# Optimization experiments

Hardware: AMD Instinct MI355X
Metric: run time of the kernel (lower is better)

Reference implementation:

```python
import jax, jax.numpy as jnp
import numpy as np

VOCAB = 50001; W2V = 300; S2V = 256; HID = 256; COUT = 256; NTAG = 4; NHEADS = 5
N_POSTS = 2048; SEQ = 64


def mha(x, wqkv, bqkv, wo, bo, h):
    # torch nn.MultiheadAttention (batch_first, eval mode, no mask)
    n, s, d = x.shape
    hd = d // h
    qkv = x @ wqkv.T + bqkv                      # [n, s, 3d]
    q, k, v = jnp.split(qkv, 3, axis=-1)
    rs = lambda t: t.reshape(n, s, h, hd).transpose(0, 2, 1, 3)  # [n, h, s, hd]
    q, k, v = rs(q), rs(k), rs(v)
    att = jax.nn.softmax(jnp.einsum('nhqd,nhkd->nhqk', q, k) * (hd ** -0.5), axis=-1)
    o = jnp.einsum('nhqk,nhkd->nhqd', att, v).transpose(0, 2, 1, 3).reshape(n, s, d)
    return o @ wo.T + bo


def gcn_conv(x, ei, w, b):
    n = x.shape[0]
    loops = jnp.arange(n)
    src = jnp.concatenate([ei[0], loops])
    dst = jnp.concatenate([ei[1], loops])
    deg = jax.ops.segment_sum(jnp.ones(dst.shape[0], dtype=x.dtype), dst, num_segments=n)
    dinv = jnp.where(deg > 0, jax.lax.rsqrt(deg), 0.0)
    norm = dinv[src] * dinv[dst]                 # [E+n]
    h = x @ w.T                                  # [n, out]
    return jax.ops.segment_sum(norm[:, None] * h[src], dst, num_segments=n) + b


def gcn_branch(x, ei, root, w1, b1, w2, b2):
    # GCN.forward: conv1 -> cat root feat -> relu -> conv2 -> relu -> cat conv1 root -> mean
    n = x.shape[0]
    c1 = gcn_conv(x, ei, w1, b1)                 # [n, HID]
    post_root = jnp.broadcast_to(x[root], (n, x.shape[1]))
    c2_in = jax.nn.relu(jnp.concatenate([c1, post_root], axis=1))
    c2 = jax.nn.relu(gcn_conv(c2_in, ei, w2, b2))
    c1_root = jnp.broadcast_to(c1[root], (n, c1.shape[1]))
    feat = jnp.concatenate([c1_root, c2], axis=1)  # [n, HID+COUT]
    return jnp.mean(feat, axis=0).reshape(1, -1)


def setup_inputs() -> dict:
    key = jax.random.key(0)
    ks = jax.random.split(key, 16)
    p = lambda i, shp, sc=0.02: jax.random.normal(ks[i], shp, dtype=jnp.float32) * sc
    return {
        'nodeText': jax.random.randint(ks[0], (N_POSTS, SEQ), 0, VOCAB),
        'edgeIndexTD': jax.random.randint(ks[1], (2, N_POSTS - 1), 0, N_POSTS),
        'edgeIndexBU': jax.random.randint(ks[2], (2, N_POSTS - 1), 0, N_POSTS),
        'threadIndex': 0,
        'mission': 1,
        'embed_w': p(3, (VOCAB, W2V), 1.0),
        'in_proj_w': p(4, (3 * W2V, W2V)),
        'in_proj_b': jnp.zeros((3 * W2V,), jnp.float32),
        'out_proj_w': p(5, (W2V, W2V)),
        'out_proj_b': jnp.zeros((W2V,), jnp.float32),
        's2v_w': p(6, (S2V, W2V)),
        's2v_b': jnp.zeros((S2V,), jnp.float32),
        'td_w1': p(7, (HID, S2V)), 'td_b1': jnp.zeros((HID,), jnp.float32),
        'td_w2': p(8, (COUT, HID + S2V)), 'td_b2': jnp.zeros((COUT,), jnp.float32),
        'bu_w1': p(9, (HID, S2V)), 'bu_b1': jnp.zeros((HID,), jnp.float32),
        'bu_w2': p(10, (COUT, HID + S2V)), 'bu_b2': jnp.zeros((COUT,), jnp.float32),
        'fc_w': p(11, (NTAG, (COUT + HID) * 2)),
        'fc_b': jnp.zeros((NTAG,), jnp.float32),
    }


def reference(nodeText, edgeIndexTD, edgeIndexBU, threadIndex, mission,
              embed_w, in_proj_w, in_proj_b, out_proj_w, out_proj_b,
              s2v_w, s2v_b, td_w1, td_b1, td_w2, td_b2,
              bu_w1, bu_b1, bu_w2, bu_b2, fc_w, fc_b):
    # ABGCN.forward, mission == 1 (rumor/BiGCN path), eval mode (dropout off)
    nf = embed_w[nodeText]                                  # [N, S, W2V]
    nf = mha(nf, in_proj_w, in_proj_b, out_proj_w, out_proj_b, NHEADS)
    nf = jnp.tanh(nf @ s2v_w.T + s2v_b)                     # [N, S, S2V]
    s2v = nf[:, 0, :]                                       # first token per post
    td = gcn_branch(s2v, edgeIndexTD, threadIndex, td_w1, td_b1, td_w2, td_b2)
    bu = gcn_branch(s2v, edgeIndexBU, threadIndex, bu_w1, bu_b1, bu_w2, bu_b2)
    return jnp.concatenate([td, bu], axis=1) @ fc_w.T + fc_b  # [1, NTAG]
```

## Files before the change

### kernel.cpp

```cpp
#include <hip/hip_runtime.h>

#define NPOSTS 2048
#define SEQ 64
#define W2V 300
#define NH 5
#define HD 60
#define S2VD 256
#define HIDD 256
#define NEDGE 2047

__global__ __launch_bounds__(320) void k_q(
    const int* __restrict__ nodeText, const float* __restrict__ embed_w,
    const float* __restrict__ Wqkv, const float* __restrict__ bqkv,
    float* __restrict__ Qout)
{
    const int r0 = blockIdx.x * 16;
    const int tid = threadIdx.x;
    __shared__ float sE[16][W2V];
    for (int i = tid; i < 16 * 75; i += 320) {
        int r = i / 75, c4 = (i % 75) * 4;
        int t = nodeText[(size_t)(r0 + r) * SEQ];
        const float4 v = *reinterpret_cast<const float4*>(embed_w + (size_t)t * W2V + c4);
        sE[r][c4] = v.x; sE[r][c4 + 1] = v.y; sE[r][c4 + 2] = v.z; sE[r][c4 + 3] = v.w;
    }
    __syncthreads();
    if (tid < W2V) {
        const float* wr = Wqkv + (size_t)tid * W2V;
        float acc[16];
        float b = bqkv[tid];
        #pragma unroll
        for (int r = 0; r < 16; ++r) acc[r] = b;
        for (int c = 0; c < W2V; ++c) {
            float wv = wr[c];
            #pragma unroll
            for (int r = 0; r < 16; ++r) acc[r] = fmaf(wv, sE[r][c], acc[r]);
        }
        #pragma unroll
        for (int r = 0; r < 16; ++r) Qout[(size_t)(r0 + r) * W2V + tid] = acc[r];
    }
}

__global__ __launch_bounds__(320) void k_u(
    const float* __restrict__ Q, const float* __restrict__ Wqkv, float* __restrict__ uout)
{
    const int r0 = blockIdx.x * 16;
    const int h = blockIdx.y;
    const int tid = threadIdx.x;
    __shared__ float sQ[16][HD];
    for (int i = tid; i < 16 * HD; i += 320) {
        int r = i / HD, d = i % HD;
        sQ[r][d] = Q[(size_t)(r0 + r) * W2V + h * HD + d];
    }
    __syncthreads();
    if (tid < W2V) {
        float acc[16];
        #pragma unroll
        for (int r = 0; r < 16; ++r) acc[r] = 0.f;
        const float* wb = Wqkv + (size_t)(W2V + h * HD) * W2V + tid;
        for (int d = 0; d < HD; ++d) {
            float wv = wb[(size_t)d * W2V];
            #pragma unroll
            for (int r = 0; r < 16; ++r) acc[r] = fmaf(wv, sQ[r][d], acc[r]);
        }
        #pragma unroll
        for (int r = 0; r < 16; ++r)
            uout[(size_t)(r0 + r) * (NH * W2V) + h * W2V + tid] = acc[r];
    }
}

__global__ __launch_bounds__(256) void k_att(
    const int* __restrict__ nodeText, const float* __restrict__ embed_w,
    float* __restrict__ ue)
{
    __shared__ float sEmb[SEQ][W2V + 1];
    __shared__ int   stoks[SEQ];
    __shared__ float ssc[NH * SEQ];

    const int p = blockIdx.x;
    const int tid = threadIdx.x;

    if (tid < SEQ) stoks[tid] = nodeText[p * SEQ + tid];
    __syncthreads();

    for (int idx = tid; idx < SEQ * 75; idx += 256) {
        int r = idx / 75, c4 = (idx % 75) * 4;
        const float4 v = *reinterpret_cast<const float4*>(embed_w + (size_t)stoks[r] * W2V + c4);
        float* dst = &sEmb[r][c4];
        dst[0] = v.x; dst[1] = v.y; dst[2] = v.z; dst[3] = v.w;
    }
    __syncthreads();

    const float* urow = ue + (size_t)p * (NH * W2V);
    for (int i = tid; i < NH * SEQ; i += 256) {
        int h = i / SEQ, j = i % SEQ;
        const float4* u4 = reinterpret_cast<const float4*>(urow + h * W2V);
        const float* er = sEmb[j];
        float acc = 0.f;
        for (int c4 = 0; c4 < 75; ++c4) {
            float4 u = u4[c4];
            int c = c4 * 4;
            acc = fmaf(u.x, er[c], acc);
            acc = fmaf(u.y, er[c + 1], acc);
            acc = fmaf(u.z, er[c + 2], acc);
            acc = fmaf(u.w, er[c + 3], acc);
        }
        ssc[i] = acc * 0.12909944487358056f;
    }
    __syncthreads();

    {
        const int wave = tid >> 6, lane = tid & 63;
        for (int h = wave; h < NH; h += 4) {
            float v = ssc[h * SEQ + lane];
            float m = v;
            #pragma unroll
            for (int off = 32; off > 0; off >>= 1) m = fmaxf(m, __shfl_xor(m, off));
            float e = expf(v - m);
            float s = e;
            #pragma unroll
            for (int off = 32; off > 0; off >>= 1) s += __shfl_xor(s, off);
            ssc[h * SEQ + lane] = e / s;
        }
    }
    __syncthreads();

    float* erow = ue + (size_t)p * (NH * W2V);
    for (int i = tid; i < NH * W2V; i += 256) {
        int h = i / W2V, c = i % W2V;
        const float* att = ssc + h * SEQ;
        float acc = 0.f;
        #pragma unroll 4
        for (int j = 0; j < SEQ; ++j) acc = fmaf(att[j], sEmb[j][c], acc);
        erow[i] = acc;
    }
}

__global__ __launch_bounds__(320) void k_oms(
    const float* __restrict__ e, const float* __restrict__ Wqkv, const float* __restrict__ bqkv,
    const float* __restrict__ Wo, const float* __restrict__ bo,
    const float* __restrict__ Ws, const float* __restrict__ bs,
    float* __restrict__ s2v_out)
{
    const int r0 = blockIdx.x * 8;
    const int tid = threadIdx.x;
    __shared__ float se[8][NH * W2V];
    __shared__ float so[8][W2V];
    __shared__ float sm[8][W2V];

    for (int i = tid; i < 8 * 375; i += 320) {
        int r = i / 375, c4 = (i % 375) * 4;
        const float4 v = *reinterpret_cast<const float4*>(e + (size_t)(r0 + r) * (NH * W2V) + c4);
        float* dst = &se[r][c4];
        dst[0] = v.x; dst[1] = v.y; dst[2] = v.z; dst[3] = v.w;
    }
    __syncthreads();

    if (tid < W2V) {
        const int h = tid / HD;
        const float* wr = Wqkv + (size_t)(2 * W2V + tid) * W2V;
        float acc[8];
        float b = bqkv[2 * W2V + tid];
        #pragma unroll
        for (int r = 0; r < 8; ++r) acc[r] = b;
        for (int c = 0; c < W2V; ++c) {
            float wv = wr[c];
            #pragma unroll
            for (int r = 0; r < 8; ++r) acc[r] = fmaf(wv, se[r][h * W2V + c], acc[r]);
        }
        #pragma unroll
        for (int r = 0; r < 8; ++r) so[r][tid] = acc[r];
    }
    __syncthreads();

    if (tid < W2V) {
        const float* wr = Wo + (size_t)tid * W2V;
        float acc[8];
        float b = bo[tid];
        #pragma unroll
        for (int r = 0; r < 8; ++r) acc[r] = b;
        for (int c = 0; c < W2V; ++c) {
            float wv = wr[c];
            #pragma unroll
            for (int r = 0; r < 8; ++r) acc[r] = fmaf(wv, so[r][c], acc[r]);
        }
        #pragma unroll
        for (int r = 0; r < 8; ++r) sm[r][tid] = acc[r];
    }
    __syncthreads();

    if (tid < S2VD) {
        const float* wr = Ws + (size_t)tid * W2V;
        float acc[8];
        float b = bs[tid];
        #pragma unroll
        for (int r = 0; r < 8; ++r) acc[r] = b;
        for (int c = 0; c < W2V; ++c) {
            float wv = wr[c];
            #pragma unroll
            for (int r = 0; r < 8; ++r) acc[r] = fmaf(wv, sm[r][c], acc[r]);
        }
        #pragma unroll
        for (int r = 0; r < 8; ++r)
            s2v_out[(size_t)(r0 + r) * S2VD + tid] = tanhf(acc[r]);
    }
}


__global__ __launch_bounds__(256) void k_deg(
    const int* __restrict__ eiTD, const int* __restrict__ eiBU, int* __restrict__ deg)
{
    const int b = blockIdx.y;
    const int* ei = b ? eiBU : eiTD;
    int e = blockIdx.x * 256 + threadIdx.x;
    if (e < NEDGE) atomicAdd(&deg[b * NPOSTS + ei[NEDGE + e]], 1);
}

__global__ __launch_bounds__(256) void k_gemm1(
    const float* __restrict__ x, const float* __restrict__ wtd, const float* __restrict__ wbu,
    float* __restrict__ hout)
{
    const int b = blockIdx.y;
    const float* w = b ? wbu : wtd;
    float* outp = hout + (size_t)b * NPOSTS * HIDD;
    const int r0 = blockIdx.x * 16;
    const int tid = threadIdx.x;
    __shared__ float sx[16][S2VD];
    for (int i = tid; i < 16 * S2VD; i += 256)
        sx[i / S2VD][i % S2VD] = x[(size_t)(r0 + i / S2VD) * S2VD + (i % S2VD)];
    __syncthreads();
    float acc[16];
    #pragma unroll
    for (int r = 0; r < 16; ++r) acc[r] = 0.f;
    const float* wr = w + (size_t)tid * S2VD;
    for (int c = 0; c < S2VD; ++c) {
        float wv = wr[c];
        #pragma unroll
        for (int r = 0; r < 16; ++r) acc[r] = fmaf(wv, sx[r][c], acc[r]);
    }
    #pragma unroll
    for (int r = 0; r < 16; ++r) outp[(size_t)(r0 + r) * HIDD + tid] = acc[r];
}

__global__ __launch_bounds__(256) void k_gemm2(
    const float* __restrict__ c1, const float* __restrict__ w2td, const float* __restrict__ w2bu,
    const float* __restrict__ rootv, float* __restrict__ hout)
{
    const int b = blockIdx.y;
    const float* w = b ? w2bu : w2td;
    const float* xin = c1 + (size_t)b * NPOSTS * HIDD;
    float* outp = hout + (size_t)b * NPOSTS * HIDD;
    const int r0 = blockIdx.x * 16;
    const int tid = threadIdx.x;
    __shared__ float sx[16][HIDD];
    for (int i = tid; i < 16 * HIDD; i += 256)
        sx[i / HIDD][i % HIDD] = fmaxf(xin[(size_t)(r0 + i / HIDD) * HIDD + (i % HIDD)], 0.f);
    __syncthreads();
    float acc[16];
    const float rv = rootv[b * HIDD + tid];
    #pragma unroll
    for (int r = 0; r < 16; ++r) acc[r] = rv;
    const float* wr = w + (size_t)tid * 512;
    for (int c = 0; c < HIDD; ++c) {
        float wv = wr[c];
        #pragma unroll
        for (int r = 0; r < 16; ++r) acc[r] = fmaf(wv, sx[r][c], acc[r]);
    }
    #pragma unroll
    for (int r = 0; r < 16; ++r) outp[(size_t)(r0 + r) * HIDD + tid] = acc[r];
}

__global__ __launch_bounds__(256) void k_init(
    const float* __restrict__ h, const float* __restrict__ btd, const float* __restrict__ bbu,
    const int* __restrict__ deg, float* __restrict__ cout_)
{
    const int b = blockIdx.y, n = blockIdx.x, tid = threadIdx.x;
    const float* bias = b ? bbu : btd;
    const float* hb = h + (size_t)b * NPOSTS * HIDD;
    float* cb = cout_ + (size_t)b * NPOSTS * HIDD;
    float dinv = 1.f / (float)(deg[b * NPOSTS + n] + 1);
    cb[(size_t)n * HIDD + tid] = bias[tid] + hb[(size_t)n * HIDD + tid] * dinv;
}

__global__ __launch_bounds__(256) void k_scat(
    const int* __restrict__ eiTD, const int* __restrict__ eiBU,
    const float* __restrict__ h, const int* __restrict__ deg, float* __restrict__ cacc)
{
    const int b = blockIdx.y, e = blockIdx.x, tid = threadIdx.x;
    const int* ei = b ? eiBU : eiTD;
    const int s = ei[e], d = ei[NEDGE + e];
    const int* dg = deg + b * NPOSTS;
    float norm = rsqrtf((float)(dg[s] + 1)) * rsqrtf((float)(dg[d] + 1));
    const float* hb = h + (size_t)b * NPOSTS * HIDD;
    float* cb = cacc + (size_t)b * NPOSTS * HIDD;
    atomicAdd(&cb[(size_t)d * HIDD + tid], norm * hb[(size_t)s * HIDD + tid]);
}

__global__ __launch_bounds__(256) void k_root(
    const float* __restrict__ s2v, const float* __restrict__ c1,
    const float* __restrict__ w2td, const float* __restrict__ w2bu,
    const int* __restrict__ rootPtr, float* __restrict__ rootv, float* __restrict__ c1root)
{
    const int b = blockIdx.y, tid = threadIdx.x;
    const float* w2 = b ? w2bu : w2td;
    const int root = rootPtr[0];
    __shared__ float sx[S2VD];
    sx[tid] = fmaxf(s2v[(size_t)root * S2VD + tid], 0.f);
    __syncthreads();
    const float* cb = c1 + (size_t)b * NPOSTS * HIDD;
    c1root[b * HIDD + tid] = cb[(size_t)root * HIDD + tid];
    const float* wr = w2 + (size_t)tid * 512 + 256;
    float acc = 0.f;
    #pragma unroll 4
    for (int c = 0; c < S2VD; ++c) acc = fmaf(wr[c], sx[c], acc);
    rootv[b * HIDD + tid] = acc;
}

__global__ __launch_bounds__(256) void k_reduce(
    const float* __restrict__ cacc, float* __restrict__ msum)
{
    const int b = blockIdx.y, tid = threadIdx.x;
    const int base = blockIdx.x * 32;
    const float* cb = cacc + (size_t)b * NPOSTS * HIDD;
    float local = 0.f;
    #pragma unroll 4
    for (int r = 0; r < 32; ++r) local += fmaxf(cb[(size_t)(base + r) * HIDD + tid], 0.f);
    atomicAdd(&msum[b * HIDD + tid], local);
}

__global__ __launch_bounds__(256) void k_final(
    const float* __restrict__ c1root, const float* __restrict__ msum,
    const float* __restrict__ fc_w, const float* __restrict__ fc_b, float* __restrict__ outp)
{
    const int tid = threadIdx.x;
    __shared__ float sf[1024];
    for (int k = tid; k < 1024; k += 256) {
        int seg = k >> 8, idx = k & 255;
        float v;
        if (seg == 0)      v = c1root[idx];
        else if (seg == 1) v = msum[idx] * (1.f / (float)NPOSTS);
        else if (seg == 2) v = c1root[256 + idx];
        else               v = msum[256 + idx] * (1.f / (float)NPOSTS);
        sf[k] = v;
    }
    __syncthreads();
    const int t = tid >> 6, lane = tid & 63;
    float part = 0.f;
    for (int k = lane; k < 1024; k += 64) part = fmaf(fc_w[t * 1024 + k], sf[k], part);
    #pragma unroll
    for (int off = 32; off > 0; off >>= 1) part += __shfl_down(part, off);
    if (lane == 0) outp[t] = part + fc_b[t];
}

extern "C" void kernel_launch(void* const* d_in, const int* in_sizes, int n_in,
                              void* d_out, int out_size, void* d_ws, size_t ws_size,
                              hipStream_t stream) {
    (void)in_sizes; (void)n_in; (void)out_size; (void)ws_size;

    const int*   nodeText   = (const int*)d_in[0];
    const int*   eiTD       = (const int*)d_in[1];
    const int*   eiBU       = (const int*)d_in[2];
    const int*   threadIdxP = (const int*)d_in[3];
    const float* embed_w    = (const float*)d_in[5];
    const float* in_proj_w  = (const float*)d_in[6];
    const float* in_proj_b  = (const float*)d_in[7];
    const float* out_proj_w = (const float*)d_in[8];
    const float* out_proj_b = (const float*)d_in[9];
    const float* s2v_w      = (const float*)d_in[10];
    const float* s2v_b      = (const float*)d_in[11];
    const float* td_w1      = (const float*)d_in[12];
    const float* td_b1      = (const float*)d_in[13];
    const float* td_w2      = (const float*)d_in[14];
    const float* td_b2      = (const float*)d_in[15];
    const float* bu_w1      = (const float*)d_in[16];
    const float* bu_b1      = (const float*)d_in[17];
    const float* bu_w2      = (const float*)d_in[18];
    const float* bu_b2      = (const float*)d_in[19];
    const float* fc_w       = (const float*)d_in[20];
    const float* fc_b       = (const float*)d_in[21];
    float* outp = (float*)d_out;

    char* w = (char*)d_ws;
    int*   deg    = (int*)w;
    float* msum   = (float*)(w + 16384);
    float* rootv  = (float*)(w + 16384 + 2048);
    float* c1root = (float*)(w + 16384 + 4096);
    float* s2v    = (float*)(w + 24576);
    float* hbuf   = (float*)(w + 24576 + 2097152);
    float* cbuf   = (float*)(w + 24576 + 2097152 + 4194304);
    float* Qbuf   = (float*)(w + 24576 + 2097152 + 4194304 + 4194304);
    float* uebuf  = (float*)(w + 24576 + 2097152 + 4194304 + 4194304 + 2457600);

    hipMemsetAsync(d_ws, 0, 16384 + 2048, stream);

    k_q  <<<NPOSTS / 16, 320, 0, stream>>>(nodeText, embed_w, in_proj_w, in_proj_b, Qbuf);
    k_u  <<<dim3(NPOSTS / 16, NH), 320, 0, stream>>>(Qbuf, in_proj_w, uebuf);
    k_att<<<NPOSTS, 256, 0, stream>>>(nodeText, embed_w, uebuf);
    k_oms<<<NPOSTS / 8, 320, 0, stream>>>(uebuf, in_proj_w, in_proj_b,
                                          out_proj_w, out_proj_b, s2v_w, s2v_b, s2v);

    k_deg<<<dim3((NEDGE + 255) / 256, 2), 256, 0, stream>>>(eiTD, eiBU, deg);

    k_gemm1<<<dim3(NPOSTS / 16, 2), 256, 0, stream>>>(s2v, td_w1, bu_w1, hbuf);
    k_init<<<dim3(NPOSTS, 2), 256, 0, stream>>>(hbuf, td_b1, bu_b1, deg, cbuf);
    k_scat<<<dim3(NEDGE, 2), 256, 0, stream>>>(eiTD, eiBU, hbuf, deg, cbuf);

    k_root<<<dim3(1, 2), 256, 0, stream>>>(s2v, cbuf, td_w2, bu_w2, threadIdxP, rootv, c1root);

    k_gemm2<<<dim3(NPOSTS / 16, 2), 256, 0, stream>>>(cbuf, td_w2, bu_w2, rootv, hbuf);
    k_init<<<dim3(NPOSTS, 2), 256, 0, stream>>>(hbuf, td_b2, bu_b2, deg, cbuf);
    k_scat<<<dim3(NEDGE, 2), 256, 0, stream>>>(eiTD, eiBU, hbuf, deg, cbuf);

    k_reduce<<<dim3(NPOSTS / 32, 2), 256, 0, stream>>>(cbuf, msum);

    k_final<<<1, 256, 0, stream>>>(c1root, msum, fc_w, fc_b, outp);
}
```

Measured before the change: 345.3 us.

## Fuse Q/U projections, restructure attention kernel, fold GCN init into GEMM epilogues

Merges the query projection and the per-head key-folded projection into one kernel working on 4 posts per block, which removes the intermediate Q buffer round trip. The attention kernel is rewritten. Each wave computes token scores with register-held u vectors and shuffle reductions, softmax runs one wave per head, and the weighted sum reads embeddings directly from global memory and reduces partial sums in shared memory, instead of staging the full 64x300 embedding tile. The output/s2v kernel is retiled to 4 rows per block. The GCN self-loop and bias init moves into the GEMM epilogues, removing the k_init launches. The trade-off is that embedding rows are now read twice from global/L2, and there are more, smaller blocks.

```diff
diff --git a/kernel.cpp b/kernel.cpp
--- a/kernel.cpp
+++ b/kernel.cpp
@@ -8,130 +8,175 @@
 #define S2VD 256
 #define HIDD 256
 #define NEDGE 2047
-
-__global__ __launch_bounds__(320) void k_q(
+#define UDIM (NH * W2V)
+
+__device__ __forceinline__ float dot4(float4 a, float4 b) {
+    return fmaf(a.x, b.x, fmaf(a.y, b.y, fmaf(a.z, b.z, a.w * b.w)));
+}
+
+__global__ __launch_bounds__(320) void k_qu(
     const int* __restrict__ nodeText, const float* __restrict__ embed_w,
     const float* __restrict__ Wqkv, const float* __restrict__ bqkv,
-    float* __restrict__ Qout)
-{
-    const int r0 = blockIdx.x * 16;
-    const int tid = threadIdx.x;
-    __shared__ float sE[16][W2V];
-    for (int i = tid; i < 16 * 75; i += 320) {
-        int r = i / 75, c4 = (i % 75) * 4;
+    float* __restrict__ uout)
+{
+    const int r0 = blockIdx.x * 4;
+    const int tid = threadIdx.x;
+    __shared__ float sE[4][W2V];
+    __shared__ float sQ[4][W2V];
+
+    if (tid < 300) {
+        int r = tid / 75, c4 = (tid % 75) * 4;
         int t = nodeText[(size_t)(r0 + r) * SEQ];
         const float4 v = *reinterpret_cast<const float4*>(embed_w + (size_t)t * W2V + c4);
         sE[r][c4] = v.x; sE[r][c4 + 1] = v.y; sE[r][c4 + 2] = v.z; sE[r][c4 + 3] = v.w;
     }
     __syncthreads();
+
     if (tid < W2V) {
         const float* wr = Wqkv + (size_t)tid * W2V;
-        float acc[16];
         float b = bqkv[tid];
-        #pragma unroll
-        for (int r = 0; r < 16; ++r) acc[r] = b;
+        float a0 = b, a1 = b, a2 = b, a3 = b;
         for (int c = 0; c < W2V; ++c) {
             float wv = wr[c];
-            #pragma unroll
-            for (int r = 0; r < 16; ++r) acc[r] = fmaf(wv, sE[r][c], acc[r]);
-        }
-        #pragma unroll
-        for (int r = 0; r < 16; ++r) Qout[(size_t)(r0 + r) * W2V + tid] = acc[r];
-    }
-}
-
-__global__ __launch_bounds__(320) void k_u(
-    const float* __restrict__ Q, const float* __restrict__ Wqkv, float* __restrict__ uout)
-{
-    const int r0 = blockIdx.x * 16;
-    const int h = blockIdx.y;
-    const int tid = threadIdx.x;
-    __shared__ float sQ[16][HD];
-    for (int i = tid; i < 16 * HD; i += 320) {
-        int r = i / HD, d = i % HD;
-        sQ[r][d] = Q[(size_t)(r0 + r) * W2V + h * HD + d];
-    }
-    __syncthreads();
+            a0 = fmaf(wv, sE[0][c], a0);
+            a1 = fmaf(wv, sE[1][c], a1);
+            a2 = fmaf(wv, sE[2][c], a2);
+            a3 = fmaf(wv, sE[3][c], a3);
+        }
+        sQ[0][tid] = a0; sQ[1][tid] = a1; sQ[2][tid] = a2; sQ[3][tid] = a3;
+    }
+    __syncthreads();
+
     if (tid < W2V) {
-        float acc[16];
-        #pragma unroll
-        for (int r = 0; r < 16; ++r) acc[r] = 0.f;
-        const float* wb = Wqkv + (size_t)(W2V + h * HD) * W2V + tid;
-        for (int d = 0; d < HD; ++d) {
-            float wv = wb[(size_t)d * W2V];
-            #pragma unroll
-            for (int r = 0; r < 16; ++r) acc[r] = fmaf(wv, sQ[r][d], acc[r]);
-        }
-        #pragma unroll
-        for (int r = 0; r < 16; ++r)
-            uout[(size_t)(r0 + r) * (NH * W2V) + h * W2V + tid] = acc[r];
-    }
-}
-
-__global__ __launch_bounds__(256) void k_att(
+        for (int h = 0; h < NH; ++h) {
+            const float* wb = Wqkv + (size_t)(W2V + h * HD) * W2V + tid;
+            const float* q0 = &sQ[0][h * HD];
+            const float* q1 = &sQ[1][h * HD];
+            const float* q2 = &sQ[2][h * HD];
+            const float* q3 = &sQ[3][h * HD];
+            float a0 = 0.f, a1 = 0.f, a2 = 0.f, a3 = 0.f;
+            for (int d = 0; d < HD; ++d) {
+                float wv = wb[(size_t)d * W2V];
+                a0 = fmaf(wv, q0[d], a0);
+                a1 = fmaf(wv, q1[d], a1);
+                a2 = fmaf(wv, q2[d], a2);
+                a3 = fmaf(wv, q3[d], a3);
+            }
+            uout[(size_t)(r0 + 0) * UDIM + h * W2V + tid] = a0;
+            uout[(size_t)(r0 + 1) * UDIM + h * W2V + tid] = a1;
+            uout[(size_t)(r0 + 2) * UDIM + h * W2V + tid] = a2;
+            uout[(size_t)(r0 + 3) * UDIM + h * W2V + tid] = a3;
+        }
+    }
+}
+
+__global__ __launch_bounds__(320) void k_att(
     const int* __restrict__ nodeText, const float* __restrict__ embed_w,
     float* __restrict__ ue)
 {
-    __shared__ float sEmb[SEQ][W2V + 1];
     __shared__ int   stoks[SEQ];
     __shared__ float ssc[NH * SEQ];
+    __shared__ float part[4][75][21];
 
     const int p = blockIdx.x;
     const int tid = threadIdx.x;
+    const int wave = tid >> 6, lane = tid & 63;
 
     if (tid < SEQ) stoks[tid] = nodeText[p * SEQ + tid];
     __syncthreads();
 
-    for (int idx = tid; idx < SEQ * 75; idx += 256) {
-        int r = idx / 75, c4 = (idx % 75) * 4;
-        const float4 v = *reinterpret_cast<const float4*>(embed_w + (size_t)stoks[r] * W2V + c4);
-        float* dst = &sEmb[r][c4];
-        dst[0] = v.x; dst[1] = v.y; dst[2] = v.z; dst[3] = v.w;
-    }
-    __syncthreads();
-
-    const float* urow = ue + (size_t)p * (NH * W2V);
-    for (int i = tid; i < NH * SEQ; i += 256) {
-        int h = i / SEQ, j = i % SEQ;
-        const float4* u4 = reinterpret_cast<const float4*>(urow + h * W2V);
-        const float* er = sEmb[j];
-        float acc = 0.f;
-        for (int c4 = 0; c4 < 75; ++c4) {
-            float4 u = u4[c4];
-            int c = c4 * 4;
-            acc = fmaf(u.x, er[c], acc);
-            acc = fmaf(u.y, er[c + 1], acc);
-            acc = fmaf(u.z, er[c + 2], acc);
-            acc = fmaf(u.w, er[c + 3], acc);
-        }
-        ssc[i] = acc * 0.12909944487358056f;
+    const float4* su4 = reinterpret_cast<const float4*>(ue + (size_t)p * UDIM);
+    float4 u00 = su4[0 * 75 + lane];
+    float4 u01 = su4[1 * 75 + lane];
+    float4 u02 = su4[2 * 75 + lane];
+    float4 u03 = su4[3 * 75 + lane];
+    float4 u04 = su4[4 * 75 + lane];
+    float4 z = make_float4(0.f, 0.f, 0.f, 0.f);
+    float4 u10 = z, u11 = z, u12 = z, u13 = z, u14 = z;
+    if (lane < 11) {
+        u10 = su4[0 * 75 + 64 + lane];
+        u11 = su4[1 * 75 + 64 + lane];
+        u12 = su4[2 * 75 + 64 + lane];
+        u13 = su4[3 * 75 + 64 + lane];
+        u14 = su4[4 * 75 + 64 + lane];
+    }
+
+    const float SC = 0.12909944487358056f;
+    for (int j = wave; j < SEQ; j += 5) {
+        const float4* er = reinterpret_cast<const float4*>(embed_w + (size_t)stoks[j] * W2V);
+        const float4 a = er[lane];
+        float4 bb = z;
+        if (lane < 11) bb = er[64 + lane];
+        float s0 = dot4(a, u00) + dot4(bb, u10);
+        float s1 = dot4(a, u01) + dot4(bb, u11);
+        float s2 = dot4(a, u02) + dot4(bb, u12);
+        float s3 = dot4(a, u03) + dot4(bb, u13);
+        float s4 = dot4(a, u04) + dot4(bb, u14);
+        #pragma unroll
+        for (int off = 32; off > 0; off >>= 1) {
+            s0 += __shfl_xor(s0, off);
+            s1 += __shfl_xor(s1, off);
+            s2 += __shfl_xor(s2, off);
+            s3 += __shfl_xor(s3, off);
+            s4 += __shfl_xor(s4, off);
+        }
+        if (lane == 0) {
+            ssc[0 * SEQ + j] = s0 * SC;
+            ssc[1 * SEQ + j] = s1 * SC;
+            ssc[2 * SEQ + j] = s2 * SC;
+            ssc[3 * SEQ + j] = s3 * SC;
+            ssc[4 * SEQ + j] = s4 * SC;
+        }
     }
     __syncthreads();
 
     {
-        const int wave = tid >> 6, lane = tid & 63;
-        for (int h = wave; h < NH; h += 4) {
-            float v = ssc[h * SEQ + lane];
-            float m = v;
-            #pragma unroll
-            for (int off = 32; off > 0; off >>= 1) m = fmaxf(m, __shfl_xor(m, off));
-            float e = expf(v - m);
-            float s = e;
-            #pragma unroll
-            for (int off = 32; off > 0; off >>= 1) s += __shfl_xor(s, off);
-            ssc[h * SEQ + lane] = e / s;
-        }
-    }
-    __syncthreads();
-
-    float* erow = ue + (size_t)p * (NH * W2V);
-    for (int i = tid; i < NH * W2V; i += 256) {
-        int h = i / W2V, c = i % W2V;
-        const float* att = ssc + h * SEQ;
-        float acc = 0.f;
-        #pragma unroll 4
-        for (int j = 0; j < SEQ; ++j) acc = fmaf(att[j], sEmb[j][c], acc);
-        erow[i] = acc;
+        float v = ssc[wave * SEQ + lane];
+        float m = v;
+        #pragma unroll
+        for (int off = 32; off > 0; off >>= 1) m = fmaxf(m, __shfl_xor(m, off));
+        float e = expf(v - m);
+        float s = e;
+        #pragma unroll
+        for (int off = 32; off > 0; off >>= 1) s += __shfl_xor(s, off);
+        ssc[wave * SEQ + lane] = e / s;
+    }
+    __syncthreads();
+
+    if (tid < 300) {
+        const int c4 = tid % 75, g = tid / 75;
+        float4 a0 = z, a1 = z, a2 = z, a3 = z, a4 = z;
+        for (int jj = 0; jj < 16; ++jj) {
+            int j = g * 16 + jj;
+            const float4 em = *reinterpret_cast<const float4*>(
+                embed_w + (size_t)stoks[j] * W2V + c4 * 4);
+            float w0 = ssc[0 * SEQ + j], w1 = ssc[1 * SEQ + j], w2 = ssc[2 * SEQ + j];
+            float w3 = ssc[3 * SEQ + j], w4 = ssc[4 * SEQ + j];
+            a0.x = fmaf(w0, em.x, a0.x); a0.y = fmaf(w0, em.y, a0.y); a0.z = fmaf(w0, em.z, a0.z); a0.w = fmaf(w0, em.w, a0.w);
+            a1.x = fmaf(w1, em.x, a1.x); a1.y = fmaf(w1, em.y, a1.y); a1.z = fmaf(w1, em.z, a1.z); a1.w = fmaf(w1, em.w, a1.w);
+            a2.x = fmaf(w2, em.x, a2.x); a2.y = fmaf(w2, em.y, a2.y); a2.z = fmaf(w2, em.z, a2.z); a2.w = fmaf(w2, em.w, a2.w);
+            a3.x = fmaf(w3, em.x, a3.x); a3.y = fmaf(w3, em.y, a3.y); a3.z = fmaf(w3, em.z, a3.z); a3.w = fmaf(w3, em.w, a3.w);
+            a4.x = fmaf(w4, em.x, a4.x); a4.y = fmaf(w4, em.y, a4.y); a4.z = fmaf(w4, em.z, a4.z); a4.w = fmaf(w4, em.w, a4.w);
+        }
+        float* pp = &part[g][c4][0];
+        pp[0] = a0.x; pp[1] = a0.y; pp[2] = a0.z; pp[3] = a0.w;
+        pp[4] = a1.x; pp[5] = a1.y; pp[6] = a1.z; pp[7] = a1.w;
+        pp[8] = a2.x; pp[9] = a2.y; pp[10] = a2.z; pp[11] = a2.w;
+        pp[12] = a3.x; pp[13] = a3.y; pp[14] = a3.z; pp[15] = a3.w;
+        pp[16] = a4.x; pp[17] = a4.y; pp[18] = a4.z; pp[19] = a4.w;
+    }
+    __syncthreads();
+
+    float4* eo = reinterpret_cast<float4*>(ue + (size_t)p * UDIM);
+    for (int o = tid; o < 375; o += 320) {
+        int h = o / 75, c4 = o % 75;
+        float x = 0.f, y = 0.f, zz = 0.f, w = 0.f;
+        #pragma unroll
+        for (int g = 0; g < 4; ++g) {
+            const float* pp = &part[g][c4][h * 4];
+            x += pp[0]; y += pp[1]; zz += pp[2]; w += pp[3];
+        }
+        eo[o] = make_float4(x, y, zz, w);
     }
 }
 
@@ -141,67 +186,69 @@
     const float* __restrict__ Ws, const float* __restrict__ bs,
     float* __restrict__ s2v_out)
 {
-    const int r0 = blockIdx.x * 8;
-    const int tid = threadIdx.x;
-    __shared__ float se[8][NH * W2V];
-    __shared__ float so[8][W2V];
-    __shared__ float sm[8][W2V];
-
-    for (int i = tid; i < 8 * 375; i += 320) {
+    const int r0 = blockIdx.x * 4;
+    const int tid = threadIdx.x;
+    __shared__ float se[4][UDIM];
+    __shared__ float so[4][W2V];
+    __shared__ float sm[4][W2V];
+
+    for (int i = tid; i < 4 * 375; i += 320) {
         int r = i / 375, c4 = (i % 375) * 4;
-        const float4 v = *reinterpret_cast<const float4*>(e + (size_t)(r0 + r) * (NH * W2V) + c4);
-        float* dst = &se[r][c4];
-        dst[0] = v.x; dst[1] = v.y; dst[2] = v.z; dst[3] = v.w;
+        const float4 v = *reinterpret_cast<const float4*>(e + (size_t)(r0 + r) * UDIM + c4);
+        se[r][c4] = v.x; se[r][c4 + 1] = v.y; se[r][c4 + 2] = v.z; se[r][c4 + 3] = v.w;
     }
     __syncthreads();
 
     if (tid < W2V) {
         const int h = tid / HD;
         const float* wr = Wqkv + (size_t)(2 * W2V + tid) * W2V;
-        float acc[8];
         float b = bqkv[2 * W2V + tid];
-        #pragma unroll
-        for (int r = 0; r < 8; ++r) acc[r] = b;
+        float a0 = b, a1 = b, a2 = b, a3 = b;
+        const float* e0 = &se[0][h * W2V];
+        const float* e1 = &se[1][h * W2V];
+        const float* e2 = &se[2][h * W2V];
+        const float* e3 = &se[3][h * W2V];
         for (int c = 0; c < W2V; ++c) {
             float wv = wr[c];
-            #pragma unroll
-            for (int r = 0; r < 8; ++r) acc[r] = fmaf(wv, se[r][h * W2V + c], acc[r]);
-        }
-        #pragma unroll
-        for (int r = 0; r < 8; ++r) so[r][tid] = acc[r];
+            a0 = fmaf(wv, e0[c], a0);
+            a1 = fmaf(wv, e1[c], a1);
+            a2 = fmaf(wv, e2[c], a2);
+            a3 = fmaf(wv, e3[c], a3);
+        }
+        so[0][tid] = a0; so[1][tid] = a1; so[2][tid] = a2; so[3][tid] = a3;
     }
     __syncthreads();
 
     if (tid < W2V) {
         const float* wr = Wo + (size_t)tid * W2V;
-        float acc[8];
         float b = bo[tid];
-        #pragma unroll
-        for (int r = 0; r < 8; ++r) acc[r] = b;
+        float a0 = b, a1 = b, a2 = b, a3 = b;
         for (int c = 0; c < W2V; ++c) {
             float wv = wr[c];
-            #pragma unroll
-            for (int r = 0; r < 8; ++r) acc[r] = fmaf(wv, so[r][c], acc[r]);
-        }
-        #pragma unroll
-        for (int r = 0; r < 8; ++r) sm[r][tid] = acc[r];
+            a0 = fmaf(wv, so[0][c], a0);
+            a1 = fmaf(wv, so[1][c], a1);
+            a2 = fmaf(wv, so[2][c], a2);
+            a3 = fmaf(wv, so[3][c], a3);
+        }
+        sm[0][tid] = a0; sm[1][tid] = a1; sm[2][tid] = a2; sm[3][tid] = a3;
     }
     __syncthreads();
 
     if (tid < S2VD) {
         const float* wr = Ws + (size_t)tid * W2V;
-        float acc[8];
         float b = bs[tid];
-        #pragma unroll
-        for (int r = 0; r < 8; ++r) acc[r] = b;
+        float a0 = b, a1 = b, a2 = b, a3 = b;
         for (int c = 0; c < W2V; ++c) {
             float wv = wr[c];
-            #pragma unroll
-            for (int r = 0; r < 8; ++r) acc[r] = fmaf(wv, sm[r][c], acc[r]);
-        }
-        #pragma unroll
-        for (int r = 0; r < 8; ++r)
-            s2v_out[(size_t)(r0 + r) * S2VD + tid] = tanhf(acc[r]);
+            a0 = fmaf(wv, sm[0][c], a0);
+            a1 = fmaf(wv, sm[1][c], a1);
+            a2 = fmaf(wv, sm[2][c], a2);
+            a3 = fmaf(wv, sm[3][c], a3);
+        }
+        s2v_out[(size_t)(r0 + 0) * S2VD + tid] = tanhf(a0);
+        s2v_out[(size_t)(r0 + 1) * S2VD + tid] = tanhf(a1);
+        s2v_out[(size_t)(r0 + 2) * S2VD + tid] = tanhf(a2);
+        s2v_out[(size_t)(r0 + 3) * S2VD + tid] = tanhf(a3);
     }
 }
 
@@ -217,11 +264,15 @@
 
 __global__ __launch_bounds__(256) void k_gemm1(
     const float* __restrict__ x, const float* __restrict__ wtd, const float* __restrict__ wbu,
-    float* __restrict__ hout)
+    const float* __restrict__ btd, const float* __restrict__ bbu, const int* __restrict__ deg,
+    float* __restrict__ hout, float* __restrict__ cout_)
 {
     const int b = blockIdx.y;
     const float* w = b ? wbu : wtd;
-    float* outp = hout + (size_t)b * NPOSTS * HIDD;
+    const float* bias = b ? bbu : btd;
+    float* hb = hout + (size_t)b * NPOSTS * HIDD;
+    float* cb = cout_ + (size_t)b * NPOSTS * HIDD;
+    const int* dg = deg + b * NPOSTS;
     const int r0 = blockIdx.x * 16;
     const int tid = threadIdx.x;
     __shared__ float sx[16][S2VD];
@@ -237,18 +288,28 @@
         #pragma unroll
         for (int r = 0; r < 16; ++r) acc[r] = fmaf(wv, sx[r][c], acc[r]);
     }
+    float bv = bias[tid];
     #pragma unroll
-    for (int r = 0; r < 16; ++r) outp[(size_t)(r0 + r) * HIDD + tid] = acc[r];
+    for (int r = 0; r < 16; ++r) {
+        int n = r0 + r;
+        float dinv = 1.f / (float)(dg[n] + 1);
+        hb[(size_t)n * HIDD + tid] = acc[r];
+        cb[(size_t)n * HIDD + tid] = bv + acc[r] * dinv;
+    }
 }
 
 __global__ __launch_bounds__(256) void k_gemm2(
     const float* __restrict__ c1, const float* __restrict__ w2td, const float* __restrict__ w2bu,
-    const float* __restrict__ rootv, float* __restrict__ hout)
+    const float* __restrict__ btd, const float* __restrict__ bbu, const int* __restrict__ deg,
+    const float* __restrict__ rootv, float* __restrict__ hout, float* __restrict__ cout_)
 {
     const int b = blockIdx.y;
     const float* w = b ? w2bu : w2td;
+    const float* bias = b ? bbu : btd;
     const float* xin = c1 + (size_t)b * NPOSTS * HIDD;
-    float* outp = hout + (size_t)b * NPOSTS * HIDD;
+    float* hb = hout + (size_t)b * NPOSTS * HIDD;
+    float* cb = cout_ + (size_t)b * NPOSTS * HIDD;
+    const int* dg = deg + b * NPOSTS;
     const int r0 = blockIdx.x * 16;
     const int tid = threadIdx.x;
     __shared__ float sx[16][HIDD];
@@ -265,20 +326,14 @@
         #pragma unroll
         for (int r = 0; r < 16; ++r) acc[r] = fmaf(wv, sx[r][c], acc[r]);
     }
+    float bv = bias[tid];
     #pragma unroll
-    for (int r = 0; r < 16; ++r) outp[(size_t)(r0 + r) * HIDD + tid] = acc[r];
-}
-
-__global__ __launch_bounds__(256) void k_init(
-    const float* __restrict__ h, const float* __restrict__ btd, const float* __restrict__ bbu,
-    const int* __restrict__ deg, float* __restrict__ cout_)
-{
-    const int b = blockIdx.y, n = blockIdx.x, tid = threadIdx.x;
-    const float* bias = b ? bbu : btd;
-    const float* hb = h + (size_t)b * NPOSTS * HIDD;
-    float* cb = cout_ + (size_t)b * NPOSTS * HIDD;
-    float dinv = 1.f / (float)(deg[b * NPOSTS + n] + 1);
-    cb[(size_t)n * HIDD + tid] = bias[tid] + hb[(size_t)n * HIDD + tid] * dinv;
+    for (int r = 0; r < 16; ++r) {
+        int n = r0 + r;
+        float dinv = 1.f / (float)(dg[n] + 1);
+        hb[(size_t)n * HIDD + tid] = acc[r];
+        cb[(size_t)n * HIDD + tid] = bv + acc[r] * dinv;
+    }
 }
 
 __global__ __launch_bounds__(256) void k_scat(
@@ -387,27 +442,25 @@
     float* s2v    = (float*)(w + 24576);
     float* hbuf   = (float*)(w + 24576 + 2097152);
     float* cbuf   = (float*)(w + 24576 + 2097152 + 4194304);
-    float* Qbuf   = (float*)(w + 24576 + 2097152 + 4194304 + 4194304);
-    float* uebuf  = (float*)(w + 24576 + 2097152 + 4194304 + 4194304 + 2457600);
+    float* uebuf  = (float*)(w + 24576 + 2097152 + 4194304 + 4194304);
 
     hipMemsetAsync(d_ws, 0, 16384 + 2048, stream);
 
-    k_q  <<<NPOSTS / 16, 320, 0, stream>>>(nodeText, embed_w, in_proj_w, in_proj_b, Qbuf);
-    k_u  <<<dim3(NPOSTS / 16, NH), 320, 0, stream>>>(Qbuf, in_proj_w, uebuf);
-    k_att<<<NPOSTS, 256, 0, stream>>>(nodeText, embed_w, uebuf);
-    k_oms<<<NPOSTS / 8, 320, 0, stream>>>(uebuf, in_proj_w, in_proj_b,
+    k_deg<<<dim3((NEDGE + 255) / 256, 2), 256, 0, stream>>>(eiTD, eiBU, deg);
+
+    k_qu <<<NPOSTS / 4, 320, 0, stream>>>(nodeText, embed_w, in_proj_w, in_proj_b, uebuf);
+    k_att<<<NPOSTS, 320, 0, stream>>>(nodeText, embed_w, uebuf);
+    k_oms<<<NPOSTS / 4, 320, 0, stream>>>(uebuf, in_proj_w, in_proj_b,
                                           out_proj_w, out_proj_b, s2v_w, s2v_b, s2v);
 
-    k_deg<<<dim3((NEDGE + 255) / 256, 2), 256, 0, stream>>>(eiTD, eiBU, deg);
-
-    k_gemm1<<<dim3(NPOSTS / 16, 2), 256, 0, stream>>>(s2v, td_w1, bu_w1, hbuf);
-    k_init<<<dim3(NPOSTS, 2), 256, 0, stream>>>(hbuf, td_b1, bu_b1, deg, cbuf);
+    k_gemm1<<<dim3(NPOSTS / 16, 2), 256, 0, stream>>>(s2v, td_w1, bu_w1, td_b1, bu_b1, deg,
+                                                      hbuf, cbuf);
     k_scat<<<dim3(NEDGE, 2), 256, 0, stream>>>(eiTD, eiBU, hbuf, deg, cbuf);
 
     k_root<<<dim3(1, 2), 256, 0, stream>>>(s2v, cbuf, td_w2, bu_w2, threadIdxP, rootv, c1root);
 
-    k_gemm2<<<dim3(NPOSTS / 16, 2), 256, 0, stream>>>(cbuf, td_w2, bu_w2, rootv, hbuf);
-    k_init<<<dim3(NPOSTS, 2), 256, 0, stream>>>(hbuf, td_b2, bu_b2, deg, cbuf);
+    k_gemm2<<<dim3(NPOSTS / 16, 2), 256, 0, stream>>>(cbuf, td_w2, bu_w2, td_b2, bu_b2, deg,
+                                                      rootv, hbuf, cbuf);
     k_scat<<<dim3(NEDGE, 2), 256, 0, stream>>>(eiTD, eiBU, hbuf, deg, cbuf);
 
     k_reduce<<<dim3(NPOSTS / 32, 2), 256, 0, stream>>>(cbuf, msum);
```

Measured after the change: 289.8 us. 16.1% less time.
